# Performance work log

Measured on AMD Instinct MI355X. Metric: run time of the kernel, lower is better.

Reference implementation:

```python
import jax, jax.numpy as jnp
import numpy as np

N_STEP = 3

def setup_inputs() -> dict:
    key = jax.random.key(0)
    ks = jax.random.split(key, 5)
    bs, l, d = 16, 128, 256
    feat = jax.random.normal(ks[0], (bs, l, d), dtype=jnp.float32)
    mask = jnp.ones((bs, l), dtype=jnp.float32)
    # torch nn.Linear init scale ~ 1/sqrt(fan_in)
    agg_w = jax.random.normal(ks[1], (d, d), dtype=jnp.float32) / np.sqrt(d)
    agg_b = jnp.zeros((d,), dtype=jnp.float32)
    attn_w = jax.random.normal(ks[2], (d, 2 * d), dtype=jnp.float32) / np.sqrt(2 * d)
    attn_b = jnp.zeros((d,), dtype=jnp.float32)
    upd_w = jax.random.normal(ks[3], (d, 2 * d), dtype=jnp.float32) / np.sqrt(2 * d)
    upd_b = jnp.zeros((d,), dtype=jnp.float32)
    return {"feat": feat, "mask": mask, "agg_w": agg_w, "agg_b": agg_b,
            "attn_w": attn_w, "attn_b": attn_b, "upd_w": upd_w, "upd_b": upd_b}


def reference(feat, mask, agg_w, agg_b, attn_w, attn_b, upd_w, upd_b):
    # Faithful, vectorized version of GCNShared.forward (eval mode: dropout = identity).
    # attn(cat(xhid_i, xhid_j)) splits into xhid_i @ W1.T + xhid_j @ W2.T + b.
    bs, l, d = feat.shape
    W1 = attn_w[:, :d]   # acts on xhid (the full sequence, index i)
    W2 = attn_w[:, d:]   # acts on the broadcast query token j
    hid = feat
    for _ in range(N_STEP):
        hid = hid * mask[:, :, None]
        xhid = jnp.einsum('bid,ed->bie', hid, agg_w) + agg_b  # [bs, l, d]
        s1 = jnp.einsum('bid,ed->bie', xhid, W1)  # key-side term,  [bs, i, d]
        s2 = jnp.einsum('bjd,ed->bje', xhid, W2)  # query-side term, [bs, j, d]
        # scores[b, j, i, e]: per-feature pairwise attention logits
        scores = s1[:, None, :, :] + s2[:, :, None, :] + attn_b
        w = jax.nn.softmax(scores, axis=2)  # softmax over sequence dim i (dim=1 in torch)
        agg = jax.nn.sigmoid(jnp.einsum('bjie,bie->bje', w, xhid))  # [bs, l, d]
        xcat = jnp.concatenate([xhid, agg], axis=2)  # [bs, l, 2d]
        hid = jnp.einsum('bjf,ef->bje', xcat, upd_w) + upd_b
    return hid
```

## Files before the change

kernel.cpp:

```cpp
#include <hip/hip_runtime.h>
#include <cmath>


template<int AMODE>
__device__ __forceinline__ void gemm32(
    const float* __restrict__ Asrc, int astride, int aoff,
    const float* __restrict__ Wt, int wld, int c0,
    int r0, const float* __restrict__ maskp, const float* abL,
    const float* caL, float* As , float* Bs ,
    int t, float (&acc)[2][4])
{
    const int tx = t & 15, ty = t >> 4;
    const int ar = t >> 3, ak = (t & 7) << 2;
    const int bk = t >> 4, bc4 = (t & 15) << 2;
    const float* ap = Asrc + (size_t)(r0 + ar) * astride + aoff;
    const float mv = (AMODE != 0) ? maskp[r0 + ar] : 1.f;

    float4 va, vb0, vb1;
    va  = *(const float4*)(ap + ak);
    vb0 = *(const float4*)(Wt + (size_t)bk * wld + c0 + bc4);
    vb1 = *(const float4*)(Wt + (size_t)(bk + 16) * wld + c0 + bc4);

    for (int ch = 0; ch < 8; ++ch) {
        const int k0 = ch * 32;
        {
            float4 v = va;
            if (AMODE == 2) {
                float4 c4 = *(const float4*)(caL + k0 + ak);
                float4 b4 = *(const float4*)(abL + k0 + ak);
                v.x = fmaf(mv, v.x + c4.x, b4.x); v.y = fmaf(mv, v.y + c4.y, b4.y);
                v.z = fmaf(mv, v.z + c4.z, b4.z); v.w = fmaf(mv, v.w + c4.w, b4.w);
            }
            As[(ak + 0) * 36 + ar] = v.x; As[(ak + 1) * 36 + ar] = v.y;
            As[(ak + 2) * 36 + ar] = v.z; As[(ak + 3) * 36 + ar] = v.w;
            *(float4*)&Bs[bk * 68 + bc4] = vb0;
            *(float4*)&Bs[(bk + 16) * 68 + bc4] = vb1;
        }
        __syncthreads();
        if (ch < 7) {
            const int kn = k0 + 32;
            va  = *(const float4*)(ap + kn + ak);
            vb0 = *(const float4*)(Wt + (size_t)(kn + bk) * wld + c0 + bc4);
            vb1 = *(const float4*)(Wt + (size_t)(kn + bk + 16) * wld + c0 + bc4);
        }
        #pragma unroll
        for (int kk = 0; kk < 32; ++kk) {
            float2 a2 = *(const float2*)&As[kk * 36 + ty * 2];
            float4 bv = *(const float4*)&Bs[kk * 68 + tx * 4];
            acc[0][0]=fmaf(a2.x,bv.x,acc[0][0]); acc[0][1]=fmaf(a2.x,bv.y,acc[0][1]);
            acc[0][2]=fmaf(a2.x,bv.z,acc[0][2]); acc[0][3]=fmaf(a2.x,bv.w,acc[0][3]);
            acc[1][0]=fmaf(a2.y,bv.x,acc[1][0]); acc[1][1]=fmaf(a2.y,bv.y,acc[1][1]);
            acc[1][2]=fmaf(a2.y,bv.z,acc[1][2]); acc[1][3]=fmaf(a2.y,bv.w,acc[1][3]);
        }
        __syncthreads();
    }
}

template<int AMODE>
__device__ __forceinline__ void gemm32d(
    const float* __restrict__ Asrc, int astride,
    const float* __restrict__ Wt1, int wld1,
    const float* __restrict__ Wt2, int wld2, int c0, int r0,
    const float* __restrict__ maskp, const float* abL, const float* caL,
    float* As, float* Bs1, float* Bs2, int t,
    float (&accS)[2][4], float (&accV)[2][4])
{
    const int tx = t & 15, ty = t >> 4;
    const int ar = t >> 3, ak = (t & 7) << 2;
    const int bk = t >> 4, bc4 = (t & 15) << 2;
    const float* ap = Asrc + (size_t)(r0 + ar) * astride;
    const float mv = (AMODE != 0) ? maskp[r0 + ar] : 1.f;

    float4 va, vb0, vb1, vc0, vc1;
    va  = *(const float4*)(ap + ak);
    vb0 = *(const float4*)(Wt1 + (size_t)bk * wld1 + c0 + bc4);
    vb1 = *(const float4*)(Wt1 + (size_t)(bk + 16) * wld1 + c0 + bc4);
    vc0 = *(const float4*)(Wt2 + (size_t)bk * wld2 + c0 + bc4);
    vc1 = *(const float4*)(Wt2 + (size_t)(bk + 16) * wld2 + c0 + bc4);

    for (int ch = 0; ch < 8; ++ch) {
        const int k0 = ch * 32;
        {
            float4 v = va;
            if (AMODE == 2) {
                float4 c4 = *(const float4*)(caL + k0 + ak);
                float4 b4 = *(const float4*)(abL + k0 + ak);
                v.x = fmaf(mv, v.x + c4.x, b4.x); v.y = fmaf(mv, v.y + c4.y, b4.y);
                v.z = fmaf(mv, v.z + c4.z, b4.z); v.w = fmaf(mv, v.w + c4.w, b4.w);
            }
            As[(ak + 0) * 36 + ar] = v.x; As[(ak + 1) * 36 + ar] = v.y;
            As[(ak + 2) * 36 + ar] = v.z; As[(ak + 3) * 36 + ar] = v.w;
            *(float4*)&Bs1[bk * 68 + bc4] = vb0;
            *(float4*)&Bs1[(bk + 16) * 68 + bc4] = vb1;
            *(float4*)&Bs2[bk * 68 + bc4] = vc0;
            *(float4*)&Bs2[(bk + 16) * 68 + bc4] = vc1;
        }
        __syncthreads();
        if (ch < 7) {
            const int kn = k0 + 32;
            va  = *(const float4*)(ap + kn + ak);
            vb0 = *(const float4*)(Wt1 + (size_t)(kn + bk) * wld1 + c0 + bc4);
            vb1 = *(const float4*)(Wt1 + (size_t)(kn + bk + 16) * wld1 + c0 + bc4);
            vc0 = *(const float4*)(Wt2 + (size_t)(kn + bk) * wld2 + c0 + bc4);
            vc1 = *(const float4*)(Wt2 + (size_t)(kn + bk + 16) * wld2 + c0 + bc4);
        }
        #pragma unroll
        for (int kk = 0; kk < 32; ++kk) {
            float2 a2 = *(const float2*)&As[kk * 36 + ty * 2];
            float4 b1 = *(const float4*)&Bs1[kk * 68 + tx * 4];
            float4 b2 = *(const float4*)&Bs2[kk * 68 + tx * 4];
            accS[0][0]=fmaf(a2.x,b1.x,accS[0][0]); accS[0][1]=fmaf(a2.x,b1.y,accS[0][1]);
            accS[0][2]=fmaf(a2.x,b1.z,accS[0][2]); accS[0][3]=fmaf(a2.x,b1.w,accS[0][3]);
            accS[1][0]=fmaf(a2.y,b1.x,accS[1][0]); accS[1][1]=fmaf(a2.y,b1.y,accS[1][1]);
            accS[1][2]=fmaf(a2.y,b1.z,accS[1][2]); accS[1][3]=fmaf(a2.y,b1.w,accS[1][3]);
            accV[0][0]=fmaf(a2.x,b2.x,accV[0][0]); accV[0][1]=fmaf(a2.x,b2.y,accV[0][1]);
            accV[0][2]=fmaf(a2.x,b2.z,accV[0][2]); accV[0][3]=fmaf(a2.x,b2.w,accV[0][3]);
            accV[1][0]=fmaf(a2.y,b2.x,accV[1][0]); accV[1][1]=fmaf(a2.y,b2.y,accV[1][1]);
            accV[1][2]=fmaf(a2.y,b2.z,accV[1][2]); accV[1][3]=fmaf(a2.y,b2.w,accV[1][3]);
        }
        __syncthreads();
    }
}

template<int AMODE>
__device__ __forceinline__ void stats_epi(
    const float* __restrict__ Asrc, const float* __restrict__ maskp,
    const float* abL, const float* caL,
    int r0, int c0, int bx, int t, const float (&acc)[2][4],
    float* __restrict__ pz, float* __restrict__ pa)
{
    const int tx = t & 15, ty = t >> 4;
    const int e = c0 + tx * 4;
    float xh[2][4];
    #pragma unroll
    for (int i = 0; i < 2; ++i) {
        const int r = r0 + ty * 2 + i;
        float4 v = *(const float4*)(Asrc + (size_t)r * 256 + e);
        if (AMODE == 2) {
            const float mv = maskp[r];
            float4 c4 = *(const float4*)(caL + e);
            float4 b4 = *(const float4*)(abL + e);
            v.x = fmaf(mv, v.x + c4.x, b4.x); v.y = fmaf(mv, v.y + c4.y, b4.y);
            v.z = fmaf(mv, v.z + c4.z, b4.z); v.w = fmaf(mv, v.w + c4.w, b4.w);
        }
        xh[i][0] = v.x; xh[i][1] = v.y; xh[i][2] = v.z; xh[i][3] = v.w;
    }
    float pzv[4], pav[4];
    #pragma unroll
    for (int j = 0; j < 4; ++j) {
        float p0 = __expf(acc[0][j]), p1 = __expf(acc[1][j]);
        pzv[j] = p0 + p1;
        pav[j] = fmaf(p0, xh[0][j], p1 * xh[1][j]);
    }
    const int gg = bx * 16 + ty;
    *(float4*)(pz + (size_t)gg * 256 + e) = make_float4(pzv[0], pzv[1], pzv[2], pzv[3]);
    *(float4*)(pa + (size_t)gg * 256 + e) = make_float4(pav[0], pav[1], pav[2], pav[3]);
}

__device__ __forceinline__ void stats_pair(
    const float (&aS)[2][4], const float (&aV)[2][4],
    int c0, int bx, int t, float* __restrict__ pz, float* __restrict__ pa)
{
    const int tx = t & 15, ty = t >> 4;
    const int e = c0 + tx * 4;
    float pzv[4], pav[4];
    #pragma unroll
    for (int j = 0; j < 4; ++j) {
        float p0 = __expf(aS[0][j]), p1 = __expf(aS[1][j]);
        pzv[j] = p0 + p1;
        pav[j] = fmaf(p0, aV[0][j], p1 * aV[1][j]);
    }
    const int gg = bx * 16 + ty;
    *(float4*)(pz + (size_t)gg * 256 + e) = make_float4(pzv[0], pzv[1], pzv[2], pzv[3]);
    *(float4*)(pa + (size_t)gg * 256 + e) = make_float4(pav[0], pav[1], pav[2], pav[3]);
}

__device__ __forceinline__ void write_epi(float* __restrict__ dst, int r0, int c0,
                                          int t, const float (&acc)[2][4]) {
    const int tx = t & 15, ty = t >> 4;
    const int e = c0 + tx * 4;
    #pragma unroll
    for (int i = 0; i < 2; ++i)
        *(float4*)(dst + (size_t)(r0 + ty * 2 + i) * 256 + e) =
            make_float4(acc[i][0], acc[i][1], acc[i][2], acc[i][3]);
}

__device__ __forceinline__ void write_epiT(float* __restrict__ dst, int ld, int off,
                                           int r0, int k0, int t, const float (&acc)[2][4]) {
    const int tx = t & 15, ty = t >> 4;
    #pragma unroll
    for (int j = 0; j < 4; ++j)
        *(float2*)(dst + (size_t)(k0 + tx * 4 + j) * ld + off + r0 + ty * 2) =
            make_float2(acc[0][j], acc[1][j]);
}

__device__ inline void transp(const float* __restrict__ src, int sld, int scol0,
                              float* __restrict__ dst, int dld,
                              int ti, int tt, float* lds) {
    const int tr = (ti >> 3) * 32, tc = (ti & 7) * 32;
    const int rr = tt >> 5, cc = tt & 31;
    #pragma unroll
    for (int p = 0; p < 4; ++p) {
        int row = p * 8 + rr;
        lds[row * 33 + cc] = src[(size_t)(tr + row) * sld + scol0 + tc + cc];
    }
    __syncthreads();
    #pragma unroll
    for (int p = 0; p < 4; ++p) {
        int krow = p * 8 + rr;
        dst[(size_t)(tc + krow) * dld + tr + cc] = lds[cc * 33 + krow];
    }
    __syncthreads();
}

__global__ __launch_bounds__(256) void l0_k(
    const float* __restrict__ feat, const float* __restrict__ mask,
    const float* __restrict__ agg_w, const float* __restrict__ agg_b,
    const float* __restrict__ attn_w, const float* __restrict__ upd_w,
    const float* __restrict__ upd_b,
    float* __restrict__ wt12, float* __restrict__ u1t, float* __restrict__ u2t,
    float* __restrict__ m2t, float* __restrict__ v0, float* __restrict__ buf0)
{
    const int bid = blockIdx.x, t = threadIdx.x;
    __shared__ __align__(16) float shb[3840];
    float* As = shb; float* Bs = shb + 1152;

    if (bid < 64) {
        const int which = bid >> 5, idx = bid & 31;
        const int er = (idx >> 2) * 32, kc = (idx & 3) * 64;
        const int co = which ? 256 : 0;
        float acc[2][4] = {};
        gemm32<0>(agg_w, 256, 0, upd_w, 512, co + kc, er, nullptr, nullptr, nullptr,
                  As, Bs, t, acc);
        if (!which) write_epiT(wt12, 512, 256, er, kc, t, acc);
        else        write_epiT(m2t,  256, 0,   er, kc, t, acc);
    } else if (bid < 128) {
        transp(attn_w, 512, 0, wt12, 512, bid - 64, t, shb);
    } else if (bid < 192) {
        transp(upd_w, 512, 0, u1t, 256, bid - 128, t, shb);
    } else if (bid < 256) {
        transp(upd_w, 512, 256, u2t, 256, bid - 192, t, shb);
    } else if (bid == 256) {
        float* ub = shb;
        ub[t] = upd_b[t];
        __syncthreads();
        float acc = 0.f;
        const float* wr = agg_w + (size_t)t * 256;
        #pragma unroll 8
        for (int d = 0; d < 256; ++d) acc = fmaf(wr[d], ub[d], acc);
        v0[t] = acc;
    } else {
        const int v = bid - 257;
        const int r0 = (v & 63) * 32, e0 = (v >> 6) * 64;
        const int tx = t & 15, ty = t >> 4;
        const int ar = t >> 3, ak = (t & 7) << 2;
        const int br = t >> 2, bk4 = (t & 3) << 3;
        float acc[2][4] = {};
        for (int k0 = 0; k0 < 256; k0 += 32) {
            {
                float4 va = *(const float4*)(feat + (size_t)(r0 + ar) * 256 + k0 + ak);
                const float mv = mask[r0 + ar];
                As[(ak + 0) * 36 + ar] = va.x * mv; As[(ak + 1) * 36 + ar] = va.y * mv;
                As[(ak + 2) * 36 + ar] = va.z * mv; As[(ak + 3) * 36 + ar] = va.w * mv;
                float4 w0 = *(const float4*)(agg_w + (size_t)(e0 + br) * 256 + k0 + bk4);
                float4 w1 = *(const float4*)(agg_w + (size_t)(e0 + br) * 256 + k0 + bk4 + 4);
                Bs[(bk4 + 0) * 68 + br] = w0.x; Bs[(bk4 + 1) * 68 + br] = w0.y;
                Bs[(bk4 + 2) * 68 + br] = w0.z; Bs[(bk4 + 3) * 68 + br] = w0.w;
                Bs[(bk4 + 4) * 68 + br] = w1.x; Bs[(bk4 + 5) * 68 + br] = w1.y;
                Bs[(bk4 + 6) * 68 + br] = w1.z; Bs[(bk4 + 7) * 68 + br] = w1.w;
            }
            __syncthreads();
            #pragma unroll
            for (int kk = 0; kk < 32; ++kk) {
                float2 a2 = *(const float2*)&As[kk * 36 + ty * 2];
                float4 bv = *(const float4*)&Bs[kk * 68 + tx * 4];
                acc[0][0]=fmaf(a2.x,bv.x,acc[0][0]); acc[0][1]=fmaf(a2.x,bv.y,acc[0][1]);
                acc[0][2]=fmaf(a2.x,bv.z,acc[0][2]); acc[0][3]=fmaf(a2.x,bv.w,acc[0][3]);
                acc[1][0]=fmaf(a2.y,bv.x,acc[1][0]); acc[1][1]=fmaf(a2.y,bv.y,acc[1][1]);
                acc[1][2]=fmaf(a2.y,bv.z,acc[1][2]); acc[1][3]=fmaf(a2.y,bv.w,acc[1][3]);
            }
            __syncthreads();
        }
        const int e = e0 + tx * 4;
        float4 b4 = *(const float4*)(agg_b + e);
        #pragma unroll
        for (int i = 0; i < 2; ++i)
            *(float4*)(buf0 + (size_t)(r0 + ty * 2 + i) * 256 + e) =
                make_float4(acc[i][0] + b4.x, acc[i][1] + b4.y,
                            acc[i][2] + b4.z, acc[i][3] + b4.w);
    }
}

__global__ __launch_bounds__(256, 4) void big1_k(
    const float* __restrict__ buf0, const float* __restrict__ wt12,
    float* __restrict__ kst, float* __restrict__ buf1,
    float* __restrict__ pz0, float* __restrict__ pa0)
{
    __shared__ __align__(16) float shb[5504];
    float* As = shb; float* Bs1 = shb + 1152; float* Bs2 = shb + 3328;
    const int t = threadIdx.x;
    const int bx = blockIdx.x, by = blockIdx.y;

    if (bx >= 64) {
        const int idx = (bx - 64) * 4 + by;
        const int kr = (idx >> 2) * 32, ec = (idx & 3) * 64;
        float acc[2][4] = {};
        gemm32<0>(wt12, 512, 256, wt12, 512, ec, kr, nullptr, nullptr, nullptr,
                  As, Bs1, t, acc);
        write_epi(kst, kr, ec, t, acc);
        return;
    }

    const int r0 = bx * 32, c0 = by * 64;
    float accS[2][4] = {}, accV[2][4] = {};
    gemm32d<0>(buf0, 256, wt12, 512, wt12 + 256, 512, c0, r0,
               nullptr, nullptr, nullptr, As, Bs1, Bs2, t, accS, accV);
    stats_epi<0>(buf0, nullptr, nullptr, nullptr, r0, c0, bx, t, accS, pz0, pa0);
    write_epi(buf1, r0, c0, t, accV);
}

__global__ __launch_bounds__(1024) void ck1_k(
    const float* __restrict__ pz0, const float* __restrict__ pa0,
    const float* __restrict__ m2t, const float* __restrict__ v0,
    float* __restrict__ caG)
{
    __shared__ float zr[4][256], arr[4][256], aggL[256];
    const int tid = threadIdx.x, t = tid & 255, s = tid >> 8;
    const int b = blockIdx.x;
    float z = 0.f, a = 0.f;
    #pragma unroll
    for (int g = 16 * s; g < 16 * s + 16; ++g) {
        size_t idx = (size_t)(b * 64 + g) * 256 + t;
        z += pz0[idx]; a += pa0[idx];
    }
    zr[s][t] = z; arr[s][t] = a;
    __syncthreads();
    if (s == 0) {
        z = (zr[0][t] + zr[1][t]) + (zr[2][t] + zr[3][t]);
        a = (arr[0][t] + arr[1][t]) + (arr[2][t] + arr[3][t]);
        aggL[t] = 1.f / (1.f + __expf(-(a / z)));
    }
    __syncthreads();
    float ca = 0.f;
    #pragma unroll 8
    for (int d = 64 * s; d < 64 * s + 64; ++d)
        ca = fmaf(aggL[d], m2t[(size_t)d * 256 + t], ca);
    zr[s][t] = ca;
    __syncthreads();
    if (s == 0)
        caG[b * 256 + t] = v0[t] + (zr[0][t] + zr[1][t]) + (zr[2][t] + zr[3][t]);
}

__global__ __launch_bounds__(256, 4) void big2_k(
    const float* __restrict__ buf1, const float* __restrict__ wt12,
    const float* __restrict__ kst, const float* __restrict__ caG,
    const float* __restrict__ mask, const float* __restrict__ agg_b,
    float* __restrict__ buf0,
    float* __restrict__ pz1, float* __restrict__ pa1,
    float* __restrict__ pz2, float* __restrict__ pa2)
{
    __shared__ __align__(16) float shb[6016];
    float* As = shb; float* Bs1 = shb + 1152; float* Bs2 = shb + 3328;
    float* caL = shb + 5504; float* abL = shb + 5760;

    const int t = threadIdx.x;
    const int bx = blockIdx.x, by = blockIdx.y;
    const int r0 = bx * 32, b = bx >> 2;

    caL[t] = caG[b * 256 + t];
    abL[t] = agg_b[t];
    __syncthreads();

    if (by < 4) {
        const int c0 = by * 64;
        float acc[2][4] = {};
        gemm32<2>(buf1, 256, 0, wt12, 512, c0, r0, mask, abL, caL, As, Bs1, t, acc);
        stats_epi<2>(buf1, mask, abL, caL, r0, c0, bx, t, acc, pz1, pa1);
    } else {
        const int c0 = (by - 4) * 64;
        float accS[2][4] = {}, accV[2][4] = {};
        gemm32d<2>(buf1, 256, kst, 256, wt12 + 256, 512, c0, r0,
                   mask, abL, caL, As, Bs1, Bs2, t, accS, accV);
        write_epi(buf0, r0, c0, t, accV);
        stats_pair(accS, accV, c0, bx, t, pz2, pa2);
    }
}

__global__ __launch_bounds__(1024) void ck2_k(
    const float* __restrict__ pz1, const float* __restrict__ pa1,
    const float* __restrict__ pz2, const float* __restrict__ pa2,
    const float* __restrict__ m2t, const float* __restrict__ u2t,
    const float* __restrict__ v0, const float* __restrict__ agg_b,
    const float* __restrict__ upd_b,
    float* __restrict__ caG2, float* __restrict__ c3G)
{
    __shared__ float zr[4][256], arr[4][256], aggL[256], caL[256], a3L[256];
    const int tid = threadIdx.x, t = tid & 255, s = tid >> 8;
    const int b = blockIdx.x;

    float z = 0.f, a = 0.f;
    #pragma unroll
    for (int g = 16 * s; g < 16 * s + 16; ++g) {
        size_t idx = (size_t)(b * 64 + g) * 256 + t;
        z += pz1[idx]; a += pa1[idx];
    }
    zr[s][t] = z; arr[s][t] = a;
    __syncthreads();
    if (s == 0) {
        z = (zr[0][t] + zr[1][t]) + (zr[2][t] + zr[3][t]);
        a = (arr[0][t] + arr[1][t]) + (arr[2][t] + arr[3][t]);
        aggL[t] = 1.f / (1.f + __expf(-(a / z)));
    }
    __syncthreads();
    float ca = 0.f;
    #pragma unroll 8
    for (int d = 64 * s; d < 64 * s + 64; ++d)
        ca = fmaf(aggL[d], m2t[(size_t)d * 256 + t], ca);
    zr[s][t] = ca;
    __syncthreads();
    if (s == 0) {
        float c = v0[t] + (zr[0][t] + zr[1][t]) + (zr[2][t] + zr[3][t]);
        caL[t] = c;
        caG2[b * 256 + t] = c;
    }
    __syncthreads();
    z = 0.f; a = 0.f;
    #pragma unroll
    for (int g = 16 * s; g < 16 * s + 16; ++g) {
        size_t idx = (size_t)(b * 64 + g) * 256 + t;
        z += pz2[idx]; a += pa2[idx];
    }
    zr[s][t] = z; arr[s][t] = a;
    __syncthreads();
    if (s == 0) {
        z = (zr[0][t] + zr[1][t]) + (zr[2][t] + zr[3][t]);
        a = (arr[0][t] + arr[1][t]) + (arr[2][t] + arr[3][t]);
        float A3 = a / z + caL[t] + agg_b[t];
        a3L[t] = 1.f / (1.f + __expf(-A3));
    }
    __syncthreads();
    float c3 = 0.f;
    #pragma unroll 8
    for (int d = 64 * s; d < 64 * s + 64; ++d)
        c3 = fmaf(a3L[d], u2t[(size_t)d * 256 + t], c3);
    zr[s][t] = c3;
    __syncthreads();
    if (s == 0)
        c3G[b * 256 + t] = upd_b[t] + (zr[0][t] + zr[1][t]) + (zr[2][t] + zr[3][t]);
}

__global__ __launch_bounds__(256) void big3_k(
    const float* __restrict__ buf0, const float* __restrict__ u1t,
    const float* __restrict__ caG2, const float* __restrict__ c3G,
    const float* __restrict__ mask, const float* __restrict__ agg_b,
    float* __restrict__ outp)
{
    __shared__ __align__(16) float shb[3840];
    float* As = shb; float* Bs = shb + 1152;
    float* caL = shb + 3328; float* abL = shb + 3584;

    const int t = threadIdx.x;
    const int bx = blockIdx.x, by = blockIdx.y;
    const int r0 = bx * 32, b = bx >> 2;
    const int c0 = by * 64;

    caL[t] = caG2[b * 256 + t];
    abL[t] = agg_b[t];
    __syncthreads();

    float acc[2][4] = {};
    gemm32<2>(buf0, 256, 0, u1t, 256, c0, r0, mask, abL, caL, As, Bs, t, acc);

    const int tx = t & 15, ty = t >> 4;
    const int e = c0 + tx * 4;
    float4 cc = *(const float4*)(c3G + b * 256 + e);
    #pragma unroll
    for (int i = 0; i < 2; ++i)
        *(float4*)(outp + (size_t)(r0 + ty * 2 + i) * 256 + e) =
            make_float4(acc[i][0] + cc.x, acc[i][1] + cc.y,
                        acc[i][2] + cc.z, acc[i][3] + cc.w);
}

extern "C" void kernel_launch(void* const* d_in, const int* in_sizes, int n_in,
                              void* d_out, int out_size, void* d_ws, size_t ws_size,
                              hipStream_t stream) {
    const float* feat   = (const float*)d_in[0];
    const float* mask   = (const float*)d_in[1];
    const float* agg_w  = (const float*)d_in[2];
    const float* agg_b  = (const float*)d_in[3];
    const float* attn_w = (const float*)d_in[4];
    const float* upd_w  = (const float*)d_in[6];
    const float* upd_b  = (const float*)d_in[7];
    float* out = (float*)d_out;

    float* p    = (float*)d_ws;
    float* wt12 = p; p += 256 * 512;
    float* u1t  = p; p += 256 * 256;
    float* u2t  = p; p += 256 * 256;
    float* m2t  = p; p += 256 * 256;
    float* kst  = p; p += 256 * 256;
    float* v0   = p; p += 256;
    float* buf0 = p; p += 2048 * 256;
    float* buf1 = p; p += 2048 * 256;
    float* pz0  = p; p += 1024 * 256;
    float* pa0  = p; p += 1024 * 256;
    float* pz1  = p; p += 1024 * 256;
    float* pa1  = p; p += 1024 * 256;
    float* pz2  = p; p += 1024 * 256;
    float* pa2  = p; p += 1024 * 256;
    float* caG  = p; p += 16 * 256;
    float* caG2 = p; p += 16 * 256;
    float* c3G  = p; p += 16 * 256;

    l0_k<<<513, 256, 0, stream>>>(feat, mask, agg_w, agg_b, attn_w, upd_w, upd_b,
                                  wt12, u1t, u2t, m2t, v0, buf0);
    big1_k<<<dim3(72, 4), 256, 0, stream>>>(buf0, wt12, kst, buf1, pz0, pa0);
    ck1_k<<<16, 1024, 0, stream>>>(pz0, pa0, m2t, v0, caG);
    big2_k<<<dim3(64, 8), 256, 0, stream>>>(buf1, wt12, kst, caG, mask, agg_b,
                                            buf0, pz1, pa1, pz2, pa2);
    ck2_k<<<16, 1024, 0, stream>>>(pz1, pa1, pz2, pa2, m2t, u2t, v0, agg_b, upd_b,
                                   caG2, c3G);
    big3_k<<<dim3(64, 4), 256, 0, stream>>>(buf0, u1t, caG2, c3G, mask, agg_b, out);
}
```

Measured before the change: 84.54 us.

## Fold final update GEMM into step-two kernel via precomposed weight product

Adds a precomputed product of the attention-side weight and the update weight (umt) in big1's spare blocks. big2 gains extra column blocks that apply this composed weight directly to buf1, producing the row-dependent part of the output. ck2 folds the per-batch constant terms (the agg-bias contribution through u1t plus the sigmoid aggregate through u2t) into one vector and writes the final output. This removes the big3 launch and its dependent GEMM pass at the cost of a wider big2 grid, an extra output buffer round-trip, and a slightly different floating-point association.

```diff
diff --git a/kernel.cpp b/kernel.cpp
--- a/kernel.cpp
+++ b/kernel.cpp
@@ -293,7 +293,8 @@
 
 __global__ __launch_bounds__(256, 4) void big1_k(
     const float* __restrict__ buf0, const float* __restrict__ wt12,
-    float* __restrict__ kst, float* __restrict__ buf1,
+    const float* __restrict__ u1t,
+    float* __restrict__ kst, float* __restrict__ umt, float* __restrict__ buf1,
     float* __restrict__ pz0, float* __restrict__ pa0)
 {
     __shared__ __align__(16) float shb[5504];
@@ -303,11 +304,18 @@
 
     if (bx >= 64) {
         const int idx = (bx - 64) * 4 + by;
-        const int kr = (idx >> 2) * 32, ec = (idx & 3) * 64;
+        const int half = idx >> 5, sub = idx & 31;
+        const int kr = (sub >> 2) * 32, ec = (sub & 3) * 64;
         float acc[2][4] = {};
-        gemm32<0>(wt12, 512, 256, wt12, 512, ec, kr, nullptr, nullptr, nullptr,
-                  As, Bs1, t, acc);
-        write_epi(kst, kr, ec, t, acc);
+        if (!half) {
+            gemm32<0>(wt12, 512, 256, wt12, 512, ec, kr, nullptr, nullptr, nullptr,
+                      As, Bs1, t, acc);
+            write_epi(kst, kr, ec, t, acc);
+        } else {
+            gemm32<0>(wt12, 512, 256, u1t, 256, ec, kr, nullptr, nullptr, nullptr,
+                      As, Bs1, t, acc);
+            write_epi(umt, kr, ec, t, acc);
+        }
         return;
     }
 
@@ -353,9 +361,10 @@
 
 __global__ __launch_bounds__(256, 4) void big2_k(
     const float* __restrict__ buf1, const float* __restrict__ wt12,
-    const float* __restrict__ kst, const float* __restrict__ caG,
+    const float* __restrict__ kst, const float* __restrict__ umt,
+    const float* __restrict__ caG,
     const float* __restrict__ mask, const float* __restrict__ agg_b,
-    float* __restrict__ buf0,
+    float* __restrict__ obuf,
     float* __restrict__ pz1, float* __restrict__ pa1,
     float* __restrict__ pz2, float* __restrict__ pa2)
 {
@@ -376,25 +385,31 @@
         float acc[2][4] = {};
         gemm32<2>(buf1, 256, 0, wt12, 512, c0, r0, mask, abL, caL, As, Bs1, t, acc);
         stats_epi<2>(buf1, mask, abL, caL, r0, c0, bx, t, acc, pz1, pa1);
-    } else {
+    } else if (by < 8) {
         const int c0 = (by - 4) * 64;
         float accS[2][4] = {}, accV[2][4] = {};
         gemm32d<2>(buf1, 256, kst, 256, wt12 + 256, 512, c0, r0,
                    mask, abL, caL, As, Bs1, Bs2, t, accS, accV);
-        write_epi(buf0, r0, c0, t, accV);
         stats_pair(accS, accV, c0, bx, t, pz2, pa2);
+    } else {
+        const int c0 = (by - 8) * 64;
+        float acc[2][4] = {};
+        gemm32<2>(buf1, 256, 0, umt, 256, c0, r0, mask, abL, caL, As, Bs1, t, acc);
+        write_epi(obuf, r0, c0, t, acc);
     }
 }
 
 __global__ __launch_bounds__(1024) void ck2_k(
     const float* __restrict__ pz1, const float* __restrict__ pa1,
     const float* __restrict__ pz2, const float* __restrict__ pa2,
-    const float* __restrict__ m2t, const float* __restrict__ u2t,
+    const float* __restrict__ m2t, const float* __restrict__ u1t,
+    const float* __restrict__ u2t,
     const float* __restrict__ v0, const float* __restrict__ agg_b,
     const float* __restrict__ upd_b,
-    float* __restrict__ caG2, float* __restrict__ c3G)
-{
-    __shared__ float zr[4][256], arr[4][256], aggL[256], caL[256], a3L[256];
+    const float* __restrict__ obuf, float* __restrict__ outp)
+{
+    __shared__ float zr[4][256], arr[4][256];
+    __shared__ float aggL[256], x2L[256], a3L[256], cvL[256];
     const int tid = threadIdx.x, t = tid & 255, s = tid >> 8;
     const int b = blockIdx.x;
 
@@ -418,11 +433,8 @@
         ca = fmaf(aggL[d], m2t[(size_t)d * 256 + t], ca);
     zr[s][t] = ca;
     __syncthreads();
-    if (s == 0) {
-        float c = v0[t] + (zr[0][t] + zr[1][t]) + (zr[2][t] + zr[3][t]);
-        caL[t] = c;
-        caG2[b * 256 + t] = c;
-    }
+    if (s == 0)
+        x2L[t] = v0[t] + (zr[0][t] + zr[1][t]) + (zr[2][t] + zr[3][t]) + agg_b[t];
     __syncthreads();
     z = 0.f; a = 0.f;
     #pragma unroll
@@ -435,50 +447,32 @@
     if (s == 0) {
         z = (zr[0][t] + zr[1][t]) + (zr[2][t] + zr[3][t]);
         a = (arr[0][t] + arr[1][t]) + (arr[2][t] + arr[3][t]);
-        float A3 = a / z + caL[t] + agg_b[t];
-        a3L[t] = 1.f / (1.f + __expf(-A3));
-    }
-    __syncthreads();
-    float c3 = 0.f;
+        a3L[t] = 1.f / (1.f + __expf(-(a / z + x2L[t])));
+    }
+    __syncthreads();
+    float c3 = 0.f, cu = 0.f;
     #pragma unroll 8
-    for (int d = 64 * s; d < 64 * s + 64; ++d)
+    for (int d = 64 * s; d < 64 * s + 64; ++d) {
         c3 = fmaf(a3L[d], u2t[(size_t)d * 256 + t], c3);
-    zr[s][t] = c3;
+        cu = fmaf(x2L[d], u1t[(size_t)d * 256 + t], cu);
+    }
+    zr[s][t] = c3; arr[s][t] = cu;
     __syncthreads();
     if (s == 0)
-        c3G[b * 256 + t] = upd_b[t] + (zr[0][t] + zr[1][t]) + (zr[2][t] + zr[3][t]);
-}
-
-__global__ __launch_bounds__(256) void big3_k(
-    const float* __restrict__ buf0, const float* __restrict__ u1t,
-    const float* __restrict__ caG2, const float* __restrict__ c3G,
-    const float* __restrict__ mask, const float* __restrict__ agg_b,
-    float* __restrict__ outp)
-{
-    __shared__ __align__(16) float shb[3840];
-    float* As = shb; float* Bs = shb + 1152;
-    float* caL = shb + 3328; float* abL = shb + 3584;
-
-    const int t = threadIdx.x;
-    const int bx = blockIdx.x, by = blockIdx.y;
-    const int r0 = bx * 32, b = bx >> 2;
-    const int c0 = by * 64;
-
-    caL[t] = caG2[b * 256 + t];
-    abL[t] = agg_b[t];
-    __syncthreads();
-
-    float acc[2][4] = {};
-    gemm32<2>(buf0, 256, 0, u1t, 256, c0, r0, mask, abL, caL, As, Bs, t, acc);
-
-    const int tx = t & 15, ty = t >> 4;
-    const int e = c0 + tx * 4;
-    float4 cc = *(const float4*)(c3G + b * 256 + e);
-    #pragma unroll
-    for (int i = 0; i < 2; ++i)
-        *(float4*)(outp + (size_t)(r0 + ty * 2 + i) * 256 + e) =
-            make_float4(acc[i][0] + cc.x, acc[i][1] + cc.y,
-                        acc[i][2] + cc.z, acc[i][3] + cc.w);
+        cvL[t] = upd_b[t]
+               + (zr[0][t] + zr[1][t]) + (zr[2][t] + zr[3][t])
+               + (arr[0][t] + arr[1][t]) + (arr[2][t] + arr[3][t]);
+    __syncthreads();
+    #pragma unroll
+    for (int it = 0; it < 8; ++it) {
+        int idx = it * 1024 + tid;
+        int r = idx >> 6, c4 = (idx & 63) * 4;
+        size_t off = (size_t)(b * 128 + r) * 256 + c4;
+        float4 o = *(const float4*)(obuf + off);
+        float4 cv = *(const float4*)&cvL[c4];
+        *(float4*)(outp + off) = make_float4(o.x + cv.x, o.y + cv.y,
+                                             o.z + cv.z, o.w + cv.w);
+    }
 }
 
 extern "C" void kernel_launch(void* const* d_in, const int* in_sizes, int n_in,
@@ -499,9 +493,11 @@
     float* u2t  = p; p += 256 * 256;
     float* m2t  = p; p += 256 * 256;
     float* kst  = p; p += 256 * 256;
+    float* umt  = p; p += 256 * 256;
     float* v0   = p; p += 256;
     float* buf0 = p; p += 2048 * 256;
     float* buf1 = p; p += 2048 * 256;
+    float* obuf = p; p += 2048 * 256;
     float* pz0  = p; p += 1024 * 256;
     float* pa0  = p; p += 1024 * 256;
     float* pz1  = p; p += 1024 * 256;
@@ -509,16 +505,14 @@
     float* pz2  = p; p += 1024 * 256;
     float* pa2  = p; p += 1024 * 256;
     float* caG  = p; p += 16 * 256;
-    float* caG2 = p; p += 16 * 256;
-    float* c3G  = p; p += 16 * 256;
 
     l0_k<<<513, 256, 0, stream>>>(feat, mask, agg_w, agg_b, attn_w, upd_w, upd_b,
                                   wt12, u1t, u2t, m2t, v0, buf0);
-    big1_k<<<dim3(72, 4), 256, 0, stream>>>(buf0, wt12, kst, buf1, pz0, pa0);
+    big1_k<<<dim3(80, 4), 256, 0, stream>>>(buf0, wt12, u1t, kst, umt, buf1,
+                                            pz0, pa0);
     ck1_k<<<16, 1024, 0, stream>>>(pz0, pa0, m2t, v0, caG);
-    big2_k<<<dim3(64, 8), 256, 0, stream>>>(buf1, wt12, kst, caG, mask, agg_b,
-                                            buf0, pz1, pa1, pz2, pa2);
-    ck2_k<<<16, 1024, 0, stream>>>(pz1, pa1, pz2, pa2, m2t, u2t, v0, agg_b, upd_b,
-                                   caG2, c3G);
-    big3_k<<<dim3(64, 4), 256, 0, stream>>>(buf0, u1t, caG2, c3G, mask, agg_b, out);
-}
+    big2_k<<<dim3(64, 12), 256, 0, stream>>>(buf1, wt12, kst, umt, caG, mask, agg_b,
+                                             obuf, pz1, pa1, pz2, pa2);
+    ck2_k<<<16, 1024, 0, stream>>>(pz1, pa1, pz2, pa2, m2t, u1t, u2t, v0, agg_b,
+                                   upd_b, obuf, out);
+}
```

Result: no change. 84.43 us (-0.1%).
